# Kernel tuning notes

Measured on AMD Instinct MI355X. Metric: run time of the kernel, lower is better.

## Reference

```python
import jax, jax.numpy as jnp
import numpy as np


def _chamfer_one(x, y):
    # x: [N,3], y: [M,3]; squared-Euclidean pairwise distances via norm expansion
    x2 = jnp.sum(x * x, axis=-1)  # [N]
    y2 = jnp.sum(y * y, axis=-1)  # [M]
    cross = jnp.einsum('nd,md->nm', x, y)  # [N,M]
    d = x2[:, None] + y2[None, :] - 2.0 * cross  # [N,M] squared distances
    # kaolin chamfer_distance: mean of NN sq-dists in both directions, summed (w1=w2=1)
    return jnp.mean(jnp.min(d, axis=1)) + jnp.mean(jnp.min(d, axis=0))


def reference(x, y):
    # x, y: [B, N, 3] / [B, M, 3]
    per_sample = jax.vmap(_chamfer_one)(x, y)  # [B]
    return jnp.mean(per_sample)


def setup_inputs() -> dict:
    key = jax.random.key(0)
    kx, ky = jax.random.split(key)
    x = jax.random.normal(kx, (16, 4096, 3), dtype=jnp.float32)
    y = jax.random.normal(ky, (16, 4096, 3), dtype=jnp.float32)
    return {"x": x, "y": y}
```

## Files before the change

### kernel.cpp

```cpp
#include <hip/hip_runtime.h>
#include <hip/hip_fp16.h>
#include <math.h>


typedef _Float16 f16x8  __attribute__((ext_vector_type(8)));
typedef float    f32x16 __attribute__((ext_vector_type(16)));

constexpr int BATCH = 16;
constexpr int NPTS  = 4096;
constexpr int NDB   = 2 * BATCH;
constexpr int BN    = BATCH * NPTS;
constexpr int TILES = NPTS / 32;

__global__ void __launch_bounds__(256)
prep(const float* __restrict__ x, const float* __restrict__ y,
     f16x8* __restrict__ ta, f16x8* __restrict__ qb, float* __restrict__ out) {
    int i = blockIdx.x * 256 + threadIdx.x;
    if (i == 0) out[0] = 0.0f;
    if (i >= 2 * BN) return;
    int src = i >> 16;
    int rem = i & (BN - 1);
    const float* S = src ? y : x;
    float a = S[3 * rem], b = S[3 * rem + 1], c = S[3 * rem + 2];
    _Float16 ha = (_Float16)a, hb = (_Float16)b, hc = (_Float16)c;
    float fa = (float)ha, fb = (float)hb, fc = (float)hc;
    float ss = fa * fa + fb * fb + fc * fc;
    _Float16 shi = (_Float16)ss;
    _Float16 slo = (_Float16)(ss - (float)shi);
    const _Float16 one = (_Float16)1.0f, zz = (_Float16)0.0f;
    f16x8 t = { (_Float16)(-2.0f * fa), (_Float16)(-2.0f * fb),
                (_Float16)(-2.0f * fc), shi, slo, one, one, zz };
    f16x8 q = { ha, hb, hc, one, one, shi, slo, zz };
    ta[(size_t)(1 - src) * BN + rem] = t;
    qb[(size_t)src       * BN + rem] = q;
}

__global__ void __launch_bounds__(256, 4)
chamfer_mfma(const f16x8* __restrict__ ta, const f16x8* __restrict__ qb,
             float* __restrict__ out) {
    const int bid  = blockIdx.x;
    const int qgrp = bid & 31;
    const int db   = bid >> 5;
    const int lane = threadIdx.x & 63;
    const int wave = threadIdx.x >> 6;
    const int m    = lane & 31;

    const int qtile = qgrp * 4 + wave;
    const f16x8 bfrag = qb[(size_t)db * NPTS + qtile * 32 + m];
    const f16x8* abase = ta + (size_t)db * NPTS;

    const f32x16 z = {0.0f, 0.0f, 0.0f, 0.0f, 0.0f, 0.0f, 0.0f, 0.0f,
                      0.0f, 0.0f, 0.0f, 0.0f, 0.0f, 0.0f, 0.0f, 0.0f};
    float acc0 = INFINITY, acc1 = INFINITY;

    #pragma unroll 4
    for (int tt = 0; tt < TILES; ++tt) {
        f16x8 af = abase[tt * 32 + m];
        f32x16 d = __builtin_amdgcn_mfma_f32_32x32x16_f16(af, bfrag, z, 0, 0, 0);
        acc0 = fminf(fminf(d[0],  d[1]),  acc0);
        acc1 = fminf(fminf(d[8],  d[9]),  acc1);
        acc0 = fminf(fminf(d[2],  d[3]),  acc0);
        acc1 = fminf(fminf(d[10], d[11]), acc1);
        acc0 = fminf(fminf(d[4],  d[5]),  acc0);
        acc1 = fminf(fminf(d[12], d[13]), acc1);
        acc0 = fminf(fminf(d[6],  d[7]),  acc0);
        acc1 = fminf(fminf(d[14], d[15]), acc1);
    }
    float acc = fminf(acc0, acc1);

    acc = fminf(acc, __shfl_xor(acc, 32, 64));
    #pragma unroll
    for (int off = 1; off < 64; off <<= 1) acc += __shfl_xor(acc, off, 64);

    __shared__ float s4[4];
    if (lane == 0) s4[wave] = acc;
    __syncthreads();
    if (threadIdx.x == 0) {
        float b = (s4[0] + s4[1]) + (s4[2] + s4[3]);
        atomicAdd(out, b * (0.25f / ((float)BATCH * (float)NPTS)));
    }
}

extern "C" void kernel_launch(void* const* d_in, const int* in_sizes, int n_in,
                              void* d_out, int out_size, void* d_ws, size_t ws_size,
                              hipStream_t stream) {
    const float* x = (const float*)d_in[0];
    const float* y = (const float*)d_in[1];
    float* out = (float*)d_out;

    f16x8* ta = (f16x8*)d_ws;
    f16x8* qb = ta + (size_t)NDB * NPTS;

    hipLaunchKernelGGL(prep, dim3((2 * BN + 255) / 256), dim3(256), 0, stream,
                       x, y, ta, qb, out);
    hipLaunchKernelGGL(chamfer_mfma, dim3(NDB * 32), dim3(256), 0, stream,
                       ta, qb, out);
}
```

Baseline: 86.44 us.

## Fuse fp16 point preparation into MFMA chamfer kernel with LDS staging

Removes the separate prep kernel. The main kernel now converts query points and chunks of the opposite cloud to fp16 fragments on the fly, staging them in shared memory in 1024-point chunks. The global atomicAdd is replaced by per-block partial sums reduced in a small finalize kernel. This avoids writing and reading the workspace fragments, but every block redoes the conversion of the full opposite cloud and adds barriers per chunk.

```diff
diff --git a/kernel.cpp b/kernel.cpp
--- a/kernel.cpp
+++ b/kernel.cpp
@@ -6,65 +6,87 @@
 typedef _Float16 f16x8  __attribute__((ext_vector_type(8)));
 typedef float    f32x16 __attribute__((ext_vector_type(16)));
 
-constexpr int BATCH = 16;
-constexpr int NPTS  = 4096;
-constexpr int NDB   = 2 * BATCH;
-constexpr int BN    = BATCH * NPTS;
-constexpr int TILES = NPTS / 32;
+constexpr int BATCH  = 16;
+constexpr int NPTS   = 4096;
+constexpr int NDB    = 2 * BATCH;
+constexpr int CHUNK  = 1024;
+constexpr int NCHUNK = NPTS / CHUNK;
+constexpr int NBLK   = NDB * 32;
 
-__global__ void __launch_bounds__(256)
-prep(const float* __restrict__ x, const float* __restrict__ y,
-     f16x8* __restrict__ ta, f16x8* __restrict__ qb, float* __restrict__ out) {
-    int i = blockIdx.x * 256 + threadIdx.x;
-    if (i == 0) out[0] = 0.0f;
-    if (i >= 2 * BN) return;
-    int src = i >> 16;
-    int rem = i & (BN - 1);
-    const float* S = src ? y : x;
-    float a = S[3 * rem], b = S[3 * rem + 1], c = S[3 * rem + 2];
-    _Float16 ha = (_Float16)a, hb = (_Float16)b, hc = (_Float16)c;
+__device__ __forceinline__ void cvt_point(float a, float b, float c,
+                                          _Float16& ha, _Float16& hb,
+                                          _Float16& hc, _Float16& shi,
+                                          _Float16& slo) {
+    ha = (_Float16)a; hb = (_Float16)b; hc = (_Float16)c;
     float fa = (float)ha, fb = (float)hb, fc = (float)hc;
     float ss = fa * fa + fb * fb + fc * fc;
-    _Float16 shi = (_Float16)ss;
-    _Float16 slo = (_Float16)(ss - (float)shi);
-    const _Float16 one = (_Float16)1.0f, zz = (_Float16)0.0f;
-    f16x8 t = { (_Float16)(-2.0f * fa), (_Float16)(-2.0f * fb),
-                (_Float16)(-2.0f * fc), shi, slo, one, one, zz };
-    f16x8 q = { ha, hb, hc, one, one, shi, slo, zz };
-    ta[(size_t)(1 - src) * BN + rem] = t;
-    qb[(size_t)src       * BN + rem] = q;
+    shi = (_Float16)ss;
+    slo = (_Float16)(ss - (float)shi);
 }
 
 __global__ void __launch_bounds__(256, 4)
-chamfer_mfma(const f16x8* __restrict__ ta, const f16x8* __restrict__ qb,
-             float* __restrict__ out) {
+chamfer_fused(const float* __restrict__ x, const float* __restrict__ y,
+              float* __restrict__ partial) {
     const int bid  = blockIdx.x;
     const int qgrp = bid & 31;
     const int db   = bid >> 5;
+    const int dir  = db >> 4;
+    const int batch = db & (BATCH - 1);
     const int lane = threadIdx.x & 63;
     const int wave = threadIdx.x >> 6;
     const int m    = lane & 31;
 
-    const int qtile = qgrp * 4 + wave;
-    const f16x8 bfrag = qb[(size_t)db * NPTS + qtile * 32 + m];
-    const f16x8* abase = ta + (size_t)db * NPTS;
+    const float* P  = dir ? y : x;
+    const float* G  = dir ? x : y;
+    const float* Pb = P + (size_t)batch * NPTS * 3;
+    const float* Gb = G + (size_t)batch * NPTS * 3;
+
+    const _Float16 one = (_Float16)1.0f, zz = (_Float16)0.0f;
+    f16x8 bfrag;
+    {
+        int qi = (qgrp * 4 + wave) * 32 + m;
+        _Float16 ha, hb, hc, shi, slo;
+        cvt_point(Pb[3 * qi], Pb[3 * qi + 1], Pb[3 * qi + 2],
+                  ha, hb, hc, shi, slo);
+        bfrag = (f16x8){ ha, hb, hc, one, one, shi, slo, zz };
+    }
+
+    __shared__ f16x8 As[CHUNK];
 
     const f32x16 z = {0.0f, 0.0f, 0.0f, 0.0f, 0.0f, 0.0f, 0.0f, 0.0f,
                       0.0f, 0.0f, 0.0f, 0.0f, 0.0f, 0.0f, 0.0f, 0.0f};
     float acc0 = INFINITY, acc1 = INFINITY;
 
-    #pragma unroll 4
-    for (int tt = 0; tt < TILES; ++tt) {
-        f16x8 af = abase[tt * 32 + m];
-        f32x16 d = __builtin_amdgcn_mfma_f32_32x32x16_f16(af, bfrag, z, 0, 0, 0);
-        acc0 = fminf(fminf(d[0],  d[1]),  acc0);
-        acc1 = fminf(fminf(d[8],  d[9]),  acc1);
-        acc0 = fminf(fminf(d[2],  d[3]),  acc0);
-        acc1 = fminf(fminf(d[10], d[11]), acc1);
-        acc0 = fminf(fminf(d[4],  d[5]),  acc0);
-        acc1 = fminf(fminf(d[12], d[13]), acc1);
-        acc0 = fminf(fminf(d[6],  d[7]),  acc0);
-        acc1 = fminf(fminf(d[14], d[15]), acc1);
+    for (int ch = 0; ch < NCHUNK; ++ch) {
+        __syncthreads();
+        #pragma unroll
+        for (int r = 0; r < CHUNK / 256; ++r) {
+            int s = r * 256 + threadIdx.x;
+            int j = ch * CHUNK + s;
+            _Float16 ha, hb, hc, shi, slo;
+            cvt_point(Gb[3 * j], Gb[3 * j + 1], Gb[3 * j + 2],
+                      ha, hb, hc, shi, slo);
+            As[s] = (f16x8){ (_Float16)(-2.0f * (float)ha),
+                             (_Float16)(-2.0f * (float)hb),
+                             (_Float16)(-2.0f * (float)hc),
+                             shi, slo, one, one, zz };
+        }
+        __syncthreads();
+
+        #pragma unroll 4
+        for (int tt = 0; tt < CHUNK / 32; ++tt) {
+            f16x8 af = As[tt * 32 + m];
+            f32x16 d = __builtin_amdgcn_mfma_f32_32x32x16_f16(af, bfrag, z,
+                                                              0, 0, 0);
+            acc0 = fminf(fminf(d[0],  d[1]),  acc0);
+            acc1 = fminf(fminf(d[8],  d[9]),  acc1);
+            acc0 = fminf(fminf(d[2],  d[3]),  acc0);
+            acc1 = fminf(fminf(d[10], d[11]), acc1);
+            acc0 = fminf(fminf(d[4],  d[5]),  acc0);
+            acc1 = fminf(fminf(d[12], d[13]), acc1);
+            acc0 = fminf(fminf(d[6],  d[7]),  acc0);
+            acc1 = fminf(fminf(d[14], d[15]), acc1);
+        }
     }
     float acc = fminf(acc0, acc1);
 
@@ -75,9 +97,22 @@
     __shared__ float s4[4];
     if (lane == 0) s4[wave] = acc;
     __syncthreads();
+    if (threadIdx.x == 0)
+        partial[bid] = (s4[0] + s4[1]) + (s4[2] + s4[3]);
+}
+
+__global__ void __launch_bounds__(256)
+finalize(const float* __restrict__ partial, float* __restrict__ out) {
+    float s = partial[threadIdx.x] + partial[threadIdx.x + 256] +
+              partial[threadIdx.x + 512] + partial[threadIdx.x + 768];
+    #pragma unroll
+    for (int off = 32; off > 0; off >>= 1) s += __shfl_down(s, off, 64);
+    __shared__ float ws_s[4];
+    if ((threadIdx.x & 63) == 0) ws_s[threadIdx.x >> 6] = s;
+    __syncthreads();
     if (threadIdx.x == 0) {
-        float b = (s4[0] + s4[1]) + (s4[2] + s4[3]);
-        atomicAdd(out, b * (0.25f / ((float)BATCH * (float)NPTS)));
+        float b = (ws_s[0] + ws_s[1]) + (ws_s[2] + ws_s[3]);
+        out[0] = b * (0.25f / ((float)BATCH * (float)NPTS));
     }
 }
 
@@ -87,12 +122,9 @@
     const float* x = (const float*)d_in[0];
     const float* y = (const float*)d_in[1];
     float* out = (float*)d_out;
+    float* partial = (float*)d_ws;
 
-    f16x8* ta = (f16x8*)d_ws;
-    f16x8* qb = ta + (size_t)NDB * NPTS;
-
-    hipLaunchKernelGGL(prep, dim3((2 * BN + 255) / 256), dim3(256), 0, stream,
-                       x, y, ta, qb, out);
-    hipLaunchKernelGGL(chamfer_mfma, dim3(NDB * 32), dim3(256), 0, stream,
-                       ta, qb, out);
+    hipLaunchKernelGGL(chamfer_fused, dim3(NBLK), dim3(256), 0, stream,
+                       x, y, partial);
+    hipLaunchKernelGGL(finalize, dim3(1), dim3(256), 0, stream, partial, out);
 }
```

Measured after the change: 75.02 us. -13.2%, faster.
